# Optimization experiments

Hardware: AMD Instinct MI355X
Metric: run time of the kernel (lower is better)

Reference implementation:

```python
import jax, jax.numpy as jnp
import numpy as np

T, C, H, W, D = 100, 2, 128, 128, 8192


def setup_inputs() -> dict:
    key = jax.random.key(0)
    k1, k2, k3, k4 = jax.random.split(key, 4)
    # event histogram: nonnegative intensities per (time, polarity, y, x)
    hist = jax.random.uniform(k1, (T, C, H, W), dtype=jnp.float32)
    # torchhd Random(vsa='MAP') tables are random bipolar {-1,+1} vectors
    time_w = jnp.sign(jax.random.normal(k2, (T, D), dtype=jnp.float32))
    pol_w = jnp.sign(jax.random.normal(k3, (C, D), dtype=jnp.float32))
    pos_w = jnp.sign(jax.random.normal(k4, (H * W, D), dtype=jnp.float32))
    return {"hist": hist, "time_w": time_w, "pol_w": pol_w, "pos_w": pos_w}


def reference(hist, time_w, pol_w, pos_w):
    # Original: for every nonzero pixel, bind (elementwise mul in MAP)
    # pos_hv * pol_hv * time_hv, scale by intensity, accumulate, then sign.
    # Equivalent fused form:
    #   out_d = sign( sum_{t,p,n} hist[t,p,n] * pos_w[n,d] * pol_w[p,d] * time_w[t,d] )
    t, c, h, w = hist.shape
    flat = hist.reshape(t, c, h * w)                      # [T, 2, H*W]
    # intensity-weighted sum of position HVs per (t, p): one GEMM over H*W
    acc = jnp.einsum('tpn,nd->tpd', flat, pos_w)          # [T, 2, D]
    # bind with polarity and time HVs, reduce over t and p
    gesture = jnp.einsum('tpd,pd,td->d', acc, pol_w, time_w)  # [D]
    return jnp.sign(gesture)
```

## Files before the change

### kernel.cpp

```cpp
#include <hip/hip_runtime.h>
#include <cstdint>
#include <cstddef>

#define TT    100
#define MROWS 200
#define KDIM  16384
#define DDIM  8192
#define KSL   16
#define KPER  (KDIM / KSL)

typedef __bf16 bf16x8 __attribute__((ext_vector_type(8)));
typedef float  f32x4  __attribute__((ext_vector_type(4)));

__global__ __launch_bounds__(256) void zero_kernel(float* __restrict__ out) {
    out[blockIdx.x * 256 + threadIdx.x] = 0.f;
}

static __device__ __forceinline__ void split_row(const float4 a, const float4 b,
                                                 uint4& hi, uint4& lo) {
    const float v[8] = {a.x, a.y, a.z, a.w, b.x, b.y, b.z, b.w};
    unsigned int h[8];
    unsigned int m[8];
#pragma unroll
    for (int i = 0; i < 8; ++i) {
        unsigned int u = __float_as_uint(v[i]);
        h[i] = (u + 0x8000u) & 0xFFFF0000u;
        float l = v[i] - __uint_as_float(h[i]);
        m[i] = (__float_as_uint(l) + 0x8000u) & 0xFFFF0000u;
    }
    hi.x = (h[0] >> 16) | h[1];  hi.y = (h[2] >> 16) | h[3];
    hi.z = (h[4] >> 16) | h[5];  hi.w = (h[6] >> 16) | h[7];
    lo.x = (m[0] >> 16) | m[1];  lo.y = (m[2] >> 16) | m[3];
    lo.z = (m[4] >> 16) | m[5];  lo.w = (m[6] >> 16) | m[7];
}

__global__ __launch_bounds__(256) void gemm_kernel(const float* __restrict__ hist,
                                                   const float* __restrict__ pos,
                                                   const float* __restrict__ time_w,
                                                   const float* __restrict__ pol_w,
                                                   float* __restrict__ out) {
    __shared__ alignas(16) unsigned short As[2][128][32];
    __shared__ alignas(16) unsigned short Bs[128][40];
    __shared__ float sPart[128];

    const int t     = threadIdx.x;
    const int n0    = blockIdx.x * 128;
    const int m0    = blockIdx.y * 128;
    const int kbase = blockIdx.z * KPER;

    const int lane = t & 63;
    const int wv   = t >> 6;
    const int wm   = (wv & 1) * 64;
    const int wn   = (wv >> 1) * 64;
    const int l15  = lane & 15;
    const int q8   = (lane >> 4) * 8;

    if (t < 128) sPart[t] = 0.f;

    const int ar  = t >> 2;
    const int akb = (t & 3) * 8;
    const bool v0 = (m0 + ar)      < MROWS;
    const bool v1 = (m0 + ar + 64) < MROWS;
    const float* gA0 = hist + (size_t)(m0 + ar)      * KDIM + akb + kbase;
    const float* gA1 = hist + (size_t)(m0 + ar + 64) * KDIM + akb + kbase;

    const int bp = t & 15;
    const int bq = t >> 4;
    const float* gB0 = pos + ((size_t)kbase + 2 * bp)     * DDIM + n0 + 4 * bq;
    const float* gB1 = pos + ((size_t)kbase + 2 * bp + 1) * DDIM + n0 + 4 * bq;

    f32x4 acc[4][4];
#pragma unroll
    for (int s = 0; s < 4; ++s)
#pragma unroll
        for (int j = 0; j < 4; ++j) acc[s][j] = (f32x4){0.f, 0.f, 0.f, 0.f};

    float4 a00 = {0,0,0,0}, a01 = {0,0,0,0}, a10 = {0,0,0,0}, a11 = {0,0,0,0};
    if (v0) { a00 = *(const float4*)(gA0);     a01 = *(const float4*)(gA0 + 4); }
    if (v1) { a10 = *(const float4*)(gA1);     a11 = *(const float4*)(gA1 + 4); }
    float4 bx0 = *(const float4*)(gB0);
    float4 bx1 = *(const float4*)(gB0 + 64);
    float4 by0 = *(const float4*)(gB1);
    float4 by1 = *(const float4*)(gB1 + 64);

    uint4 wAh0, wAl0, wAh1, wAl1;
    unsigned int wB[8];
    split_row(a00, a01, wAh0, wAl0);
    split_row(a10, a11, wAh1, wAl1);
    {
        const float x0[4] = {bx0.x, bx0.y, bx0.z, bx0.w};
        const float x1[4] = {bx1.x, bx1.y, bx1.z, bx1.w};
        const float y0[4] = {by0.x, by0.y, by0.z, by0.w};
        const float y1[4] = {by1.x, by1.y, by1.z, by1.w};
#pragma unroll
        for (int j = 0; j < 4; ++j) {
            wB[j]     = (__float_as_uint(x0[j]) >> 16) |
                        (__float_as_uint(y0[j]) & 0xFFFF0000u);
            wB[4 + j] = (__float_as_uint(x1[j]) >> 16) |
                        (__float_as_uint(y1[j]) & 0xFFFF0000u);
        }
    }

    for (int kk = 0; kk < KPER; kk += 32) {
        __syncthreads();

        *(uint4*)&As[0][ar][akb]      = wAh0;
        *(uint4*)&As[1][ar][akb]      = wAl0;
        *(uint4*)&As[0][ar + 64][akb] = wAh1;
        *(uint4*)&As[1][ar + 64][akb] = wAl1;
#pragma unroll
        for (int j = 0; j < 4; ++j) {
            *(unsigned int*)&Bs[4 * bq + j][2 * bp]      = wB[j];
            *(unsigned int*)&Bs[64 + 4 * bq + j][2 * bp] = wB[4 + j];
        }

        __syncthreads();

        const int kn = (kk + 32 < KPER) ? kk + 32 : 0;
        a00 = (float4){0,0,0,0}; a01 = a00; a10 = a00; a11 = a00;
        if (v0) { a00 = *(const float4*)(gA0 + kn);     a01 = *(const float4*)(gA0 + kn + 4); }
        if (v1) { a10 = *(const float4*)(gA1 + kn);     a11 = *(const float4*)(gA1 + kn + 4); }
        bx0 = *(const float4*)(gB0 + (size_t)kn * DDIM);
        bx1 = *(const float4*)(gB0 + (size_t)kn * DDIM + 64);
        by0 = *(const float4*)(gB1 + (size_t)kn * DDIM);
        by1 = *(const float4*)(gB1 + (size_t)kn * DDIM + 64);

        uint4 fb[4];
#pragma unroll
        for (int j = 0; j < 4; ++j)
            fb[j] = *(const uint4*)&Bs[wn + j * 16 + l15][q8];

#pragma unroll
        for (int s = 0; s < 4; ++s) {
            uint4 fa0 = *(const uint4*)&As[0][wm + s * 16 + l15][q8];
            uint4 fa1 = *(const uint4*)&As[1][wm + s * 16 + l15][q8];
#pragma unroll
            for (int j = 0; j < 4; ++j) {
                acc[s][j] = __builtin_amdgcn_mfma_f32_16x16x32_bf16(
                    __builtin_bit_cast(bf16x8, fa0),
                    __builtin_bit_cast(bf16x8, fb[j]), acc[s][j], 0, 0, 0);
                acc[s][j] = __builtin_amdgcn_mfma_f32_16x16x32_bf16(
                    __builtin_bit_cast(bf16x8, fa1),
                    __builtin_bit_cast(bf16x8, fb[j]), acc[s][j], 0, 0, 0);
            }
        }

        split_row(a00, a01, wAh0, wAl0);
        split_row(a10, a11, wAh1, wAl1);
        {
            const float x0[4] = {bx0.x, bx0.y, bx0.z, bx0.w};
            const float x1[4] = {bx1.x, bx1.y, bx1.z, bx1.w};
            const float y0[4] = {by0.x, by0.y, by0.z, by0.w};
            const float y1[4] = {by1.x, by1.y, by1.z, by1.w};
#pragma unroll
            for (int j = 0; j < 4; ++j) {
                wB[j]     = (__float_as_uint(x0[j]) >> 16) |
                            (__float_as_uint(y0[j]) & 0xFFFF0000u);
                wB[4 + j] = (__float_as_uint(x1[j]) >> 16) |
                            (__float_as_uint(y1[j]) & 0xFFFF0000u);
            }
        }
    }

    const int qrow = (lane >> 4) * 4;
#pragma unroll
    for (int j = 0; j < 4; ++j) {
        const int col = wn + j * 16 + l15;
        const int d   = n0 + col;
        const float p0 = pol_w[d];
        const float p1 = pol_w[DDIM + d];
        float part = 0.f;
#pragma unroll
        for (int s = 0; s < 4; ++s)
#pragma unroll
            for (int r = 0; r < 4; ++r) {
                const int m = m0 + wm + s * 16 + qrow + r;
                if (m < MROWS) {
                    const int tt_ = m >> 1;
                    const float w = time_w[(size_t)tt_ * DDIM + d] *
                                    ((m & 1) ? p1 : p0);
                    part += w * acc[s][j][r];
                }
            }
        atomicAdd(&sPart[col], part);
    }
    __syncthreads();
    if (t < 128) atomicAdd(out + n0 + t, sPart[t]);
}

__global__ __launch_bounds__(256) void sign_kernel(float* __restrict__ out) {
    int d = blockIdx.x * 256 + threadIdx.x;
    float s = out[d];
    out[d] = (s > 0.f) ? 1.f : ((s < 0.f) ? -1.f : 0.f);
}

extern "C" void kernel_launch(void* const* d_in, const int* in_sizes, int n_in,
                              void* d_out, int out_size, void* d_ws, size_t ws_size,
                              hipStream_t stream) {
    const float* hist   = (const float*)d_in[0];
    const float* time_w = (const float*)d_in[1];
    const float* pol_w  = (const float*)d_in[2];
    const float* pos_w  = (const float*)d_in[3];
    float* out = (float*)d_out;
    (void)d_ws; (void)ws_size;

    zero_kernel<<<DDIM / 256, 256, 0, stream>>>(out);
    gemm_kernel<<<dim3(DDIM / 128, 2, KSL), 256, 0, stream>>>(hist, pos_w, time_w, pol_w, out);
    sign_kernel<<<DDIM / 256, 256, 0, stream>>>(out);
}
```

Baseline: 871.7 us.

## Double threads per block and drop register prefetch in split-bf16 GEMM

The GEMM block grows from 256 to 512 threads, giving 8 waves each owning a 32x64 output subtile instead of 64x64. Each thread now loads one A row and one B row pair per k-step, and the global-load prefetch into registers is removed; loads are issued at the top of each iteration. This cuts per-thread registers and raises wave-level parallelism, at the cost of exposing global-load latency before each barrier that the software prefetch used to hide.

```diff
diff --git a/kernel.cpp b/kernel.cpp
--- a/kernel.cpp
+++ b/kernel.cpp
@@ -34,7 +34,7 @@
     lo.z = (m[4] >> 16) | m[5];  lo.w = (m[6] >> 16) | m[7];
 }
 
-__global__ __launch_bounds__(256) void gemm_kernel(const float* __restrict__ hist,
+__global__ __launch_bounds__(512) void gemm_kernel(const float* __restrict__ hist,
                                                    const float* __restrict__ pos,
                                                    const float* __restrict__ time_w,
                                                    const float* __restrict__ pol_w,
@@ -50,8 +50,8 @@
 
     const int lane = t & 63;
     const int wv   = t >> 6;
-    const int wm   = (wv & 1) * 64;
-    const int wn   = (wv >> 1) * 64;
+    const int wm   = (wv & 3) * 32;
+    const int wn   = (wv >> 2) * 64;
     const int l15  = lane & 15;
     const int q8   = (lane >> 4) * 8;
 
@@ -59,71 +59,46 @@
 
     const int ar  = t >> 2;
     const int akb = (t & 3) * 8;
-    const bool v0 = (m0 + ar)      < MROWS;
-    const bool v1 = (m0 + ar + 64) < MROWS;
-    const float* gA0 = hist + (size_t)(m0 + ar)      * KDIM + akb + kbase;
-    const float* gA1 = hist + (size_t)(m0 + ar + 64) * KDIM + akb + kbase;
+    const bool av = (m0 + ar) < MROWS;
+    const float* gA = hist + (size_t)(m0 + ar) * KDIM + akb + kbase;
 
     const int bp = t & 15;
     const int bq = t >> 4;
     const float* gB0 = pos + ((size_t)kbase + 2 * bp)     * DDIM + n0 + 4 * bq;
     const float* gB1 = pos + ((size_t)kbase + 2 * bp + 1) * DDIM + n0 + 4 * bq;
 
-    f32x4 acc[4][4];
+    f32x4 acc[2][4];
 #pragma unroll
-    for (int s = 0; s < 4; ++s)
+    for (int s = 0; s < 2; ++s)
 #pragma unroll
         for (int j = 0; j < 4; ++j) acc[s][j] = (f32x4){0.f, 0.f, 0.f, 0.f};
 
-    float4 a00 = {0,0,0,0}, a01 = {0,0,0,0}, a10 = {0,0,0,0}, a11 = {0,0,0,0};
-    if (v0) { a00 = *(const float4*)(gA0);     a01 = *(const float4*)(gA0 + 4); }
-    if (v1) { a10 = *(const float4*)(gA1);     a11 = *(const float4*)(gA1 + 4); }
-    float4 bx0 = *(const float4*)(gB0);
-    float4 bx1 = *(const float4*)(gB0 + 64);
-    float4 by0 = *(const float4*)(gB1);
-    float4 by1 = *(const float4*)(gB1 + 64);
+    for (int kk = 0; kk < KPER; kk += 32) {
+        float4 a0 = {0,0,0,0}, a1 = {0,0,0,0};
+        if (av) { a0 = *(const float4*)(gA + kk);  a1 = *(const float4*)(gA + kk + 4); }
+        float4 bx = *(const float4*)(gB0 + (size_t)kk * DDIM);
+        float4 by = *(const float4*)(gB1 + (size_t)kk * DDIM);
 
-    uint4 wAh0, wAl0, wAh1, wAl1;
-    unsigned int wB[8];
-    split_row(a00, a01, wAh0, wAl0);
-    split_row(a10, a11, wAh1, wAl1);
-    {
-        const float x0[4] = {bx0.x, bx0.y, bx0.z, bx0.w};
-        const float x1[4] = {bx1.x, bx1.y, bx1.z, bx1.w};
-        const float y0[4] = {by0.x, by0.y, by0.z, by0.w};
-        const float y1[4] = {by1.x, by1.y, by1.z, by1.w};
-#pragma unroll
-        for (int j = 0; j < 4; ++j) {
-            wB[j]     = (__float_as_uint(x0[j]) >> 16) |
-                        (__float_as_uint(y0[j]) & 0xFFFF0000u);
-            wB[4 + j] = (__float_as_uint(x1[j]) >> 16) |
-                        (__float_as_uint(y1[j]) & 0xFFFF0000u);
-        }
-    }
-
-    for (int kk = 0; kk < KPER; kk += 32) {
         __syncthreads();
 
-        *(uint4*)&As[0][ar][akb]      = wAh0;
-        *(uint4*)&As[1][ar][akb]      = wAl0;
-        *(uint4*)&As[0][ar + 64][akb] = wAh1;
-        *(uint4*)&As[1][ar + 64][akb] = wAl1;
+        {
+            uint4 hi, lo;
+            split_row(a0, a1, hi, lo);
+            *(uint4*)&As[0][ar][akb] = hi;
+            *(uint4*)&As[1][ar][akb] = lo;
+        }
+        {
+            const float xv[4] = {bx.x, bx.y, bx.z, bx.w};
+            const float yv[4] = {by.x, by.y, by.z, by.w};
 #pragma unroll
-        for (int j = 0; j < 4; ++j) {
-            *(unsigned int*)&Bs[4 * bq + j][2 * bp]      = wB[j];
-            *(unsigned int*)&Bs[64 + 4 * bq + j][2 * bp] = wB[4 + j];
+            for (int j = 0; j < 4; ++j) {
+                unsigned int w = (__float_as_uint(xv[j]) >> 16) |
+                                 (__float_as_uint(yv[j]) & 0xFFFF0000u);
+                *(unsigned int*)&Bs[4 * bq + j][2 * bp] = w;
+            }
         }
 
         __syncthreads();
-
-        const int kn = (kk + 32 < KPER) ? kk + 32 : 0;
-        a00 = (float4){0,0,0,0}; a01 = a00; a10 = a00; a11 = a00;
-        if (v0) { a00 = *(const float4*)(gA0 + kn);     a01 = *(const float4*)(gA0 + kn + 4); }
-        if (v1) { a10 = *(const float4*)(gA1 + kn);     a11 = *(const float4*)(gA1 + kn + 4); }
-        bx0 = *(const float4*)(gB0 + (size_t)kn * DDIM);
-        bx1 = *(const float4*)(gB0 + (size_t)kn * DDIM + 64);
-        by0 = *(const float4*)(gB1 + (size_t)kn * DDIM);
-        by1 = *(const float4*)(gB1 + (size_t)kn * DDIM + 64);
 
         uint4 fb[4];
 #pragma unroll
@@ -131,7 +106,7 @@
             fb[j] = *(const uint4*)&Bs[wn + j * 16 + l15][q8];
 
 #pragma unroll
-        for (int s = 0; s < 4; ++s) {
+        for (int s = 0; s < 2; ++s) {
             uint4 fa0 = *(const uint4*)&As[0][wm + s * 16 + l15][q8];
             uint4 fa1 = *(const uint4*)&As[1][wm + s * 16 + l15][q8];
 #pragma unroll
@@ -142,22 +117,6 @@
                 acc[s][j] = __builtin_amdgcn_mfma_f32_16x16x32_bf16(
                     __builtin_bit_cast(bf16x8, fa1),
                     __builtin_bit_cast(bf16x8, fb[j]), acc[s][j], 0, 0, 0);
-            }
-        }
-
-        split_row(a00, a01, wAh0, wAl0);
-        split_row(a10, a11, wAh1, wAl1);
-        {
-            const float x0[4] = {bx0.x, bx0.y, bx0.z, bx0.w};
-            const float x1[4] = {bx1.x, bx1.y, bx1.z, bx1.w};
-            const float y0[4] = {by0.x, by0.y, by0.z, by0.w};
-            const float y1[4] = {by1.x, by1.y, by1.z, by1.w};
-#pragma unroll
-            for (int j = 0; j < 4; ++j) {
-                wB[j]     = (__float_as_uint(x0[j]) >> 16) |
-                            (__float_as_uint(y0[j]) & 0xFFFF0000u);
-                wB[4 + j] = (__float_as_uint(x1[j]) >> 16) |
-                            (__float_as_uint(y1[j]) & 0xFFFF0000u);
             }
         }
     }
@@ -171,7 +130,7 @@
         const float p1 = pol_w[DDIM + d];
         float part = 0.f;
 #pragma unroll
-        for (int s = 0; s < 4; ++s)
+        for (int s = 0; s < 2; ++s)
 #pragma unroll
             for (int r = 0; r < 4; ++r) {
                 const int m = m0 + wm + s * 16 + qrow + r;
@@ -205,6 +164,6 @@
     (void)d_ws; (void)ws_size;
 
     zero_kernel<<<DDIM / 256, 256, 0, stream>>>(out);
-    gemm_kernel<<<dim3(DDIM / 128, 2, KSL), 256, 0, stream>>>(hist, pos_w, time_w, pol_w, out);
+    gemm_kernel<<<dim3(DDIM / 128, 2, KSL), 512, 0, stream>>>(hist, pos_w, time_w, pol_w, out);
     sign_kernel<<<DDIM / 256, 256, 0, stream>>>(out);
 }
```

After: 782.4 us. 1.11x faster.
